# Performance work log

Measured on AMD Instinct MI355X. Metric: run time of the kernel, lower is better.

The kernel has to match this reference:

```python
import jax, jax.numpy as jnp
import numpy as np

N_NODES = 100000
N_EDGES = 3200000
LEAKY_SLOPE = 0.01  # torch F.leaky_relu default


def _conv(x, W, b, src, dst):
    # DGL-style custom GCN conv: sum-aggregate neighbor features, then linear.
    msgs = x[src]                                            # [E, d_in]
    agg = jax.ops.segment_sum(msgs, dst, num_segments=N_NODES)  # [N, d_in]
    return agg @ W + b                                       # [N, d_out]


def setup_inputs() -> dict:
    key = jax.random.key(0)
    ks = jax.random.split(key, 8)
    features = jax.random.normal(ks[0], (N_NODES, 4), dtype=jnp.float32)
    src = jax.random.randint(ks[1], (N_EDGES,), 0, N_NODES, dtype=jnp.int32)
    dst = jax.random.randint(ks[2], (N_EDGES,), 0, N_NODES, dtype=jnp.int32)
    # Kaiming-ish init scale
    W1 = jax.random.normal(ks[3], (4, 64), dtype=jnp.float32) * (1.0 / np.sqrt(4))
    b1 = jnp.zeros((64,), dtype=jnp.float32)
    W2 = jax.random.normal(ks[4], (64, 64), dtype=jnp.float32) * (1.0 / np.sqrt(64))
    b2 = jnp.zeros((64,), dtype=jnp.float32)
    W5 = jax.random.normal(ks[5], (64, 3), dtype=jnp.float32) * (1.0 / np.sqrt(64))
    b5 = jnp.zeros((3,), dtype=jnp.float32)
    return {"features": features, "src": src, "dst": dst,
            "W1": W1, "b1": b1, "W2": W2, "b2": b2, "W5": W5, "b5": b5}


def reference(features, src, dst, W1, b1, W2, b2, W5, b5):
    lrelu = lambda v: jax.nn.leaky_relu(v, negative_slope=LEAKY_SLOPE)
    x = lrelu(_conv(features, W1, b1, src, dst))
    # layer2 weights are shared across 7 applications (as in the torch module)
    for _ in range(7):
        x = lrelu(_conv(x, W2, b2, src, dst))
    x = _conv(x, W5, b5, src, dst)
    return x
```

## Files before the change

### kernel.cpp

```cpp
#include <hip/hip_runtime.h>

#define N_NODES 100000
#define N_EDGES 3200000
#define SLOPE 0.01f

#define NBUCK 391
#define NBLK_B 256
#define EPB (N_EDGES / NBLK_B)
#define NGH (NBUCK * NBLK_B)
#define CAP_C 10240

typedef __attribute__((ext_vector_type(8))) short short8;
typedef __attribute__((ext_vector_type(4))) float f32x4;

static inline size_t align_up(size_t x, size_t a){ return (x + a - 1) / a * a; }

__device__ inline unsigned short f2bf(float f){
  unsigned u = __float_as_uint(f);
  u += 0x7fffu + ((u >> 16) & 1u);
  return (unsigned short)(u >> 16);
}
__device__ inline float bf2f(unsigned short s){
  return __uint_as_float(((unsigned)s) << 16);
}
__device__ inline void add2(float& a0, float& a1, unsigned u){
  a0 += __uint_as_float(u << 16);
  a1 += __uint_as_float(u & 0xffff0000u);
}


__global__ void gbhist_k(const int* __restrict__ dst, int* __restrict__ ghist){
  __shared__ int h[NBUCK];
  int tid = threadIdx.x, blk = blockIdx.x;
  for (int i = tid; i < NBUCK; i += 1024) h[i] = 0;
  __syncthreads();
  int e0 = blk * EPB;
  for (int e = e0 + tid; e < e0 + EPB; e += 1024) atomicAdd(&h[dst[e] >> 8], 1);
  __syncthreads();
  for (int i = tid; i < NBUCK; i += 1024) ghist[i * NBLK_B + blk] = h[i];
}

__global__ void scan1_k(const int* __restrict__ in, int* __restrict__ out,
                        int* __restrict__ bsums, int n){
  __shared__ int lds[256];
  int tid = threadIdx.x;
  int base = blockIdx.x * 1024 + tid * 4;
  int v0 = (base + 0 < n) ? in[base + 0] : 0;
  int v1 = (base + 1 < n) ? in[base + 1] : 0;
  int v2 = (base + 2 < n) ? in[base + 2] : 0;
  int v3 = (base + 3 < n) ? in[base + 3] : 0;
  int tsum = v0 + v1 + v2 + v3;
  lds[tid] = tsum;
  for (int off = 1; off < 256; off <<= 1){
    __syncthreads();
    int x = (tid >= off) ? lds[tid - off] : 0;
    __syncthreads();
    lds[tid] += x;
  }
  __syncthreads();
  int excl = lds[tid] - tsum;
  if (base + 0 < n) out[base + 0] = excl;
  if (base + 1 < n) out[base + 1] = excl + v0;
  if (base + 2 < n) out[base + 2] = excl + v0 + v1;
  if (base + 3 < n) out[base + 3] = excl + v0 + v1 + v2;
  if (tid == 255) bsums[blockIdx.x] = lds[255];
}

__global__ void scan2_k(int* bsums, int nb){
  int lane = threadIdx.x;
  int base = 0;
  for (int off = 0; off < nb; off += 64){
    int idx = off + lane;
    int v = (idx < nb) ? bsums[idx] : 0;
    int sc = v;
    for (int m = 1; m < 64; m <<= 1){
      int t = __shfl_up(sc, m);
      if (lane >= m) sc += t;
    }
    int total = __shfl(sc, 63);
    if (idx < nb) bsums[idx] = sc - v + base;
    base += total;
  }
}

__global__ void scan3_k(int* __restrict__ out, const int* __restrict__ bsums, int n){
  int i = blockIdx.x * 256 + threadIdx.x;
  if (i < n) out[i] += bsums[i >> 10];
}

__global__ void passB_k(const int* __restrict__ src, const int* __restrict__ dst,
                        const int* __restrict__ ghist, const int* __restrict__ goff,
                        int* __restrict__ pk){
  __shared__ int h[NBUCK];
  __shared__ int buf[EPB];
  int tid = threadIdx.x, blk = blockIdx.x;
  for (int i = tid; i < NBUCK; i += 1024) h[i] = ghist[i * NBLK_B + blk];
  __syncthreads();
  if (tid < 64){
    int base = 0;
    for (int off = 0; off < NBUCK; off += 64){
      int idx = off + tid;
      int v = (idx < NBUCK) ? h[idx] : 0;
      int sc = v;
      for (int m = 1; m < 64; m <<= 1){
        int t = __shfl_up(sc, m);
        if (tid >= m) sc += t;
      }
      int total = __shfl(sc, 63);
      if (idx < NBUCK) h[idx] = sc - v + base;
      base += total;
    }
  }
  __syncthreads();
  int e0 = blk * EPB;
  for (int e = e0 + tid; e < e0 + EPB; e += 1024){
    int d = dst[e];
    int p = atomicAdd(&h[d >> 8], 1);
    buf[p] = (src[e] << 8) | (d & 255);
  }
  __syncthreads();
  int wv = tid >> 6, ln = tid & 63;
  for (int b = wv; b < NBUCK; b += 16){
    int s0 = (b == 0) ? 0 : h[b - 1];
    int L  = h[b] - s0;
    int g0 = goff[b * NBLK_B + blk];
    for (int j = ln; j < L; j += 64) pk[g0 + j] = buf[s0 + j];
  }
}

__global__ void passC_k(const int* __restrict__ pk, const int* __restrict__ goff,
                        int* __restrict__ ssrc, int* __restrict__ row_ptr){
  __shared__ int cur[256];
  __shared__ int buf[CAP_C];
  int b = blockIdx.x, tid = threadIdx.x;
  if (tid < 256) cur[tid] = 0;
  __syncthreads();
  int s = goff[b * NBLK_B];
  int e = (b == NBUCK - 1) ? N_EDGES : goff[(b + 1) * NBLK_B];
  int cnt = e - s;
  for (int i = s + tid; i < e; i += 512) atomicAdd(&cur[pk[i] & 255], 1);
  __syncthreads();
  if (tid < 64){
    int base = 0;
    for (int off = 0; off < 256; off += 64){
      int idx = off + tid;
      int v = cur[idx];
      int sc = v;
      for (int m = 1; m < 64; m <<= 1){
        int t = __shfl_up(sc, m);
        if (tid >= m) sc += t;
      }
      int total = __shfl(sc, 63);
      cur[idx] = sc - v + base;
      base += total;
    }
  }
  __syncthreads();
  int node = b * 256 + tid;
  if (tid < 256 && node < N_NODES) row_ptr[node] = s + cur[tid];
  if (b == NBUCK - 1 && tid == 0) row_ptr[N_NODES] = N_EDGES;
  __syncthreads();
  for (int i = s + tid; i < e; i += 512){
    int v = pk[i];
    int p = atomicAdd(&cur[v & 255], 1);
    if (p < CAP_C) buf[p] = v >> 8;
    else ssrc[s + p] = v >> 8;
  }
  __syncthreads();
  int lim = (cnt < CAP_C) ? cnt : CAP_C;
  for (int i = tid; i < lim; i += 512) ssrc[s + i] = buf[i];
}

__global__ void conv1_k(const float* __restrict__ feat, const int* __restrict__ row_ptr,
                        const int* __restrict__ ssrc, const float* __restrict__ W1,
                        const float* __restrict__ b1, unsigned short* __restrict__ out){
  int gt = blockIdx.x * 256 + threadIdx.x;
  int node = gt >> 6;
  int lane = threadIdx.x & 63;
  int s = row_ptr[node], t = row_ptr[node + 1];
  float a0 = 0.f, a1 = 0.f, a2 = 0.f, a3 = 0.f;
  for (int i = s + lane; i < t; i += 64){
    int nb = ssrc[i];
    const float4 v = *(const float4*)(feat + (size_t)nb * 4);
    a0 += v.x; a1 += v.y; a2 += v.z; a3 += v.w;
  }
  for (int m = 1; m < 64; m <<= 1){
    a0 += __shfl_xor(a0, m);
    a1 += __shfl_xor(a1, m);
    a2 += __shfl_xor(a2, m);
    a3 += __shfl_xor(a3, m);
  }
  float o = b1[lane] + a0 * W1[lane] + a1 * W1[64 + lane] + a2 * W1[128 + lane] + a3 * W1[192 + lane];
  o = (o > 0.f) ? o : SLOPE * o;
  out[node * 64 + lane] = f2bf(o);
}

__global__ void mm64_k(const unsigned short* __restrict__ x, const float* __restrict__ W,
                       unsigned short* __restrict__ z){
  int lane = threadIdx.x & 63;
  int wid = (blockIdx.x * blockDim.x + threadIdx.x) >> 6;
  int nwaves = (gridDim.x * blockDim.x) >> 6;
  int r = lane & 15, g = lane >> 4;
  short8 Af[4][2];
  #pragma unroll
  for (int mb = 0; mb < 4; ++mb)
    #pragma unroll
    for (int kt = 0; kt < 2; ++kt){
      short8 f;
      #pragma unroll
      for (int j = 0; j < 8; ++j){
        int k = kt * 32 + g * 8 + j;
        f[j] = (short)f2bf(W[k * 64 + mb * 16 + r]);
      }
      Af[mb][kt] = f;
    }
  const int NT = N_NODES / 16;
  for (int t = wid; t < NT; t += nwaves){
    int base = t * 16;
    const short8 B0 = *(const short8*)(x + (size_t)(base + r) * 64 + g * 8);
    const short8 B1 = *(const short8*)(x + (size_t)(base + r) * 64 + 32 + g * 8);
    #pragma unroll
    for (int mb = 0; mb < 4; ++mb){
      f32x4 c = {0.f, 0.f, 0.f, 0.f};
      c = __builtin_amdgcn_mfma_f32_16x16x32_bf16(Af[mb][0], B0, c, 0, 0, 0);
      c = __builtin_amdgcn_mfma_f32_16x16x32_bf16(Af[mb][1], B1, c, 0, 0, 0);
      ushort4 pk4;
      pk4.x = f2bf(c[0]); pk4.y = f2bf(c[1]); pk4.z = f2bf(c[2]); pk4.w = f2bf(c[3]);
      *(ushort4*)(z + (size_t)(base + r) * 64 + mb * 16 + g * 4) = pk4;
    }
  }
}

__global__ void agg64_k(const unsigned short* __restrict__ z, const int* __restrict__ row_ptr,
                        const int* __restrict__ ssrc, const float* __restrict__ b,
                        unsigned short* __restrict__ out){
  int gt = blockIdx.x * 256 + threadIdx.x;
  int node = gt >> 6;
  int lane = threadIdx.x & 63;
  int s = row_ptr[node], cnt = row_ptr[node + 1] - s;
  int nb_l = ssrc[s + lane];
  int q = lane >> 3, o = lane & 7;
  const size_t oo = (size_t)(o << 3);
  float a0=0.f,a1=0.f,a2=0.f,a3=0.f,a4=0.f,a5=0.f,a6=0.f,a7=0.f;
  int cm1 = (cnt > 0) ? cnt - 1 : 0;
  uint4 v0, v1, v2, v3, v4, v5;
  if (cnt >  0){ int n = __shfl(nb_l, min( 0 + q, cm1)); v0 = *(const uint4*)(z + (size_t)n * 64 + oo); }
  if (cnt >  8){ int n = __shfl(nb_l, min( 8 + q, cm1)); v1 = *(const uint4*)(z + (size_t)n * 64 + oo); }
  if (cnt > 16){ int n = __shfl(nb_l, min(16 + q, cm1)); v2 = *(const uint4*)(z + (size_t)n * 64 + oo); }
  if (cnt > 24){ int n = __shfl(nb_l, min(24 + q, cm1)); v3 = *(const uint4*)(z + (size_t)n * 64 + oo); }
  if (cnt > 32){ int n = __shfl(nb_l, min(32 + q, cm1)); v4 = *(const uint4*)(z + (size_t)n * 64 + oo); }
  if (cnt > 40){ int n = __shfl(nb_l, min(40 + q, cm1)); v5 = *(const uint4*)(z + (size_t)n * 64 + oo); }
  #define ACC(V) { add2(a0,a1,V.x); add2(a2,a3,V.y); add2(a4,a5,V.z); add2(a6,a7,V.w); }
  if (cnt >  0){ if (cnt >=  8) ACC(v0) else { if ( 0 + q < cnt) ACC(v0) } }
  if (cnt >  8){ if (cnt >= 16) ACC(v1) else { if ( 8 + q < cnt) ACC(v1) } }
  if (cnt > 16){ if (cnt >= 24) ACC(v2) else { if (16 + q < cnt) ACC(v2) } }
  if (cnt > 24){ if (cnt >= 32) ACC(v3) else { if (24 + q < cnt) ACC(v3) } }
  if (cnt > 32){ if (cnt >= 40) ACC(v4) else { if (32 + q < cnt) ACC(v4) } }
  if (cnt > 40){ if (cnt >= 48) ACC(v5) else { if (40 + q < cnt) ACC(v5) } }
  #undef ACC
  for (int i = 48 + q; i < cnt; i += 8){
    int nb = ssrc[s + i];
    uint4 vv = *(const uint4*)(z + (size_t)nb * 64 + oo);
    add2(a0,a1,vv.x); add2(a2,a3,vv.y); add2(a4,a5,vv.z); add2(a6,a7,vv.w);
  }
  for (int m = 8; m < 64; m <<= 1){
    a0 += __shfl_xor(a0, m); a1 += __shfl_xor(a1, m);
    a2 += __shfl_xor(a2, m); a3 += __shfl_xor(a3, m);
    a4 += __shfl_xor(a4, m); a5 += __shfl_xor(a5, m);
    a6 += __shfl_xor(a6, m); a7 += __shfl_xor(a7, m);
  }
  if (lane < 8){
    const float4 bA = *(const float4*)(b + lane * 8);
    const float4 bB = *(const float4*)(b + lane * 8 + 4);
    float y0 = a0 + bA.x, y1 = a1 + bA.y, y2 = a2 + bA.z, y3 = a3 + bA.w;
    float y4 = a4 + bB.x, y5 = a5 + bB.y, y6 = a6 + bB.z, y7 = a7 + bB.w;
    y0 = (y0 > 0.f) ? y0 : SLOPE * y0;  y1 = (y1 > 0.f) ? y1 : SLOPE * y1;
    y2 = (y2 > 0.f) ? y2 : SLOPE * y2;  y3 = (y3 > 0.f) ? y3 : SLOPE * y3;
    y4 = (y4 > 0.f) ? y4 : SLOPE * y4;  y5 = (y5 > 0.f) ? y5 : SLOPE * y5;
    y6 = (y6 > 0.f) ? y6 : SLOPE * y6;  y7 = (y7 > 0.f) ? y7 : SLOPE * y7;
    uint4 pkd;
    pkd.x = (unsigned)f2bf(y0) | ((unsigned)f2bf(y1) << 16);
    pkd.y = (unsigned)f2bf(y2) | ((unsigned)f2bf(y3) << 16);
    pkd.z = (unsigned)f2bf(y4) | ((unsigned)f2bf(y5) << 16);
    pkd.w = (unsigned)f2bf(y6) | ((unsigned)f2bf(y7) << 16);
    *(uint4*)(out + (size_t)node * 64 + lane * 8) = pkd;
  }
}

__global__ void premult_k(const unsigned short* __restrict__ x, const float* __restrict__ W5,
                          float* __restrict__ y4){
  int gt = blockIdx.x * 256 + threadIdx.x;
  int node = gt >> 6;
  int lane = threadIdx.x & 63;
  float xv = bf2f(x[node * 64 + lane]);
  float p0 = xv * W5[lane * 3 + 0];
  float p1 = xv * W5[lane * 3 + 1];
  float p2 = xv * W5[lane * 3 + 2];
  for (int m = 1; m < 64; m <<= 1){
    p0 += __shfl_xor(p0, m);
    p1 += __shfl_xor(p1, m);
    p2 += __shfl_xor(p2, m);
  }
  if (lane == 0){
    float4 v; v.x = p0; v.y = p1; v.z = p2; v.w = 0.f;
    *(float4*)(y4 + (size_t)node * 4) = v;
  }
}

__global__ void agg3_k(const float* __restrict__ y4, const int* __restrict__ row_ptr,
                       const int* __restrict__ ssrc, const float* __restrict__ b5,
                       float* __restrict__ out){
  int gt = blockIdx.x * 256 + threadIdx.x;
  int node = gt >> 6;
  int lane = threadIdx.x & 63;
  int s = row_ptr[node], t = row_ptr[node + 1];
  int c = lane & 3;
  float acc = 0.f;
  for (int i = s + (lane >> 2); i < t; i += 16) acc += y4[(size_t)ssrc[i] * 4 + c];
  for (int m = 4; m < 64; m <<= 1) acc += __shfl_xor(acc, m);
  if (lane < 3) out[node * 3 + lane] = acc + b5[lane];
}


extern "C" void kernel_launch(void* const* d_in, const int* in_sizes, int n_in,
                              void* d_out, int out_size, void* d_ws, size_t ws_size,
                              hipStream_t stream){
  const float* feat = (const float*)d_in[0];
  const int*   src  = (const int*)d_in[1];
  const int*   dst  = (const int*)d_in[2];
  const float* W1   = (const float*)d_in[3];
  const float* b1   = (const float*)d_in[4];
  const float* W2   = (const float*)d_in[5];
  const float* b2   = (const float*)d_in[6];
  const float* W5   = (const float*)d_in[7];
  const float* b5   = (const float*)d_in[8];
  float* out = (float*)d_out;

  char* p = (char*)d_ws;
  auto carve = [&](size_t bytes) -> char* {
    char* r = p; p += align_up(bytes, 512); return r;
  };
  int*   row_ptr = (int*)carve((size_t)(N_NODES + 1) * 4);
  int*   bsums   = (int*)carve(512 * 4);
  int*   ghist   = (int*)carve((size_t)NGH * 4);
  int*   goff    = (int*)carve((size_t)NGH * 4);
  int*   ssrc    = (int*)carve(((size_t)N_EDGES + 64) * 4);
  unsigned short* bufA = (unsigned short*)carve((size_t)N_NODES * 64 * 2);
  unsigned short* bufB = (unsigned short*)carve((size_t)N_NODES * 64 * 2);
  float* y4      = (float*)carve((size_t)N_NODES * 4 * 4);
  int*   pk      = (int*)carve((size_t)N_EDGES * 4);
  unsigned short* zbuf = (unsigned short*)pk;

  gbhist_k<<<NBLK_B, 1024, 0, stream>>>(dst, ghist);
  {
    int nb = (NGH + 1023) / 1024;
    scan1_k<<<nb, 256, 0, stream>>>(ghist, goff, bsums, NGH);
    scan2_k<<<1, 64, 0, stream>>>(bsums, nb);
    scan3_k<<<(NGH + 255) / 256, 256, 0, stream>>>(goff, bsums, NGH);
  }
  passB_k<<<NBLK_B, 1024, 0, stream>>>(src, dst, ghist, goff, pk);
  passC_k<<<NBUCK, 512, 0, stream>>>(pk, goff, ssrc, row_ptr);
  hipMemsetAsync(ssrc + N_EDGES, 0, 64 * 4, stream);

  conv1_k<<<(N_NODES * 64) / 256, 256, 0, stream>>>(feat, row_ptr, ssrc, W1, b1, bufA);

  unsigned short* xin = bufA;
  unsigned short* xout = bufB;
  for (int l = 0; l < 7; ++l){
    mm64_k<<<512, 256, 0, stream>>>(xin, W2, zbuf);
    agg64_k<<<(N_NODES * 64) / 256, 256, 0, stream>>>(zbuf, row_ptr, ssrc, b2, xout);
    unsigned short* tmp = xin; xin = xout; xout = tmp;
  }

  premult_k<<<(N_NODES * 64) / 256, 256, 0, stream>>>(xin, W5, y4);
  agg3_k<<<(N_NODES * 64) / 256, 256, 0, stream>>>(y4, row_ptr, ssrc, b5, out);
}
```

Baseline: 606.5 us.

## Fuse aggregation and 64x64 MFMA matmul into one kernel per layer

Replaces the per-layer matmul-then-aggregate kernel pair with a single kernel that first gathers and sums neighbour rows, then multiplies the 16-node tile by W2 with MFMA from shared memory and applies bias plus leaky ReLU. The intermediate z buffer and one launch per layer go away. W2 is converted once into a bf16 fragment layout by a small precompute kernel. The neighbour loads are also made unconditional and clamped so they can all issue together. The cost is that only one wave of each 1024-thread block runs the MFMA after a barrier, and rounding the aggregate to bf16 before the matmul changes numerics slightly.

```diff
diff --git a/kernel.cpp b/kernel.cpp
--- a/kernel.cpp
+++ b/kernel.cpp
@@ -171,6 +171,17 @@
   for (int i = tid; i < lim; i += 512) ssrc[s + i] = buf[i];
 }
 
+__global__ void wfrag_k(const float* __restrict__ W, unsigned short* __restrict__ Wfrag){
+  int l = threadIdx.x;
+  int r = l & 15, g = l >> 4;
+  for (int mb = 0; mb < 4; ++mb)
+    for (int kt = 0; kt < 2; ++kt)
+      for (int j = 0; j < 8; ++j){
+        int k = kt * 32 + g * 8 + j;
+        Wfrag[((mb * 2 + kt) * 64 + l) * 8 + j] = f2bf(W[k * 64 + mb * 16 + r]);
+      }
+}
+
 __global__ void conv1_k(const float* __restrict__ feat, const int* __restrict__ row_ptr,
                         const int* __restrict__ ssrc, const float* __restrict__ W1,
                         const float* __restrict__ b1, unsigned short* __restrict__ out){
@@ -195,72 +206,42 @@
   out[node * 64 + lane] = f2bf(o);
 }
 
-__global__ void mm64_k(const unsigned short* __restrict__ x, const float* __restrict__ W,
-                       unsigned short* __restrict__ z){
-  int lane = threadIdx.x & 63;
-  int wid = (blockIdx.x * blockDim.x + threadIdx.x) >> 6;
-  int nwaves = (gridDim.x * blockDim.x) >> 6;
-  int r = lane & 15, g = lane >> 4;
-  short8 Af[4][2];
-  #pragma unroll
-  for (int mb = 0; mb < 4; ++mb)
-    #pragma unroll
-    for (int kt = 0; kt < 2; ++kt){
-      short8 f;
-      #pragma unroll
-      for (int j = 0; j < 8; ++j){
-        int k = kt * 32 + g * 8 + j;
-        f[j] = (short)f2bf(W[k * 64 + mb * 16 + r]);
-      }
-      Af[mb][kt] = f;
-    }
-  const int NT = N_NODES / 16;
-  for (int t = wid; t < NT; t += nwaves){
-    int base = t * 16;
-    const short8 B0 = *(const short8*)(x + (size_t)(base + r) * 64 + g * 8);
-    const short8 B1 = *(const short8*)(x + (size_t)(base + r) * 64 + 32 + g * 8);
-    #pragma unroll
-    for (int mb = 0; mb < 4; ++mb){
-      f32x4 c = {0.f, 0.f, 0.f, 0.f};
-      c = __builtin_amdgcn_mfma_f32_16x16x32_bf16(Af[mb][0], B0, c, 0, 0, 0);
-      c = __builtin_amdgcn_mfma_f32_16x16x32_bf16(Af[mb][1], B1, c, 0, 0, 0);
-      ushort4 pk4;
-      pk4.x = f2bf(c[0]); pk4.y = f2bf(c[1]); pk4.z = f2bf(c[2]); pk4.w = f2bf(c[3]);
-      *(ushort4*)(z + (size_t)(base + r) * 64 + mb * 16 + g * 4) = pk4;
-    }
-  }
-}
-
-__global__ void agg64_k(const unsigned short* __restrict__ z, const int* __restrict__ row_ptr,
-                        const int* __restrict__ ssrc, const float* __restrict__ b,
-                        unsigned short* __restrict__ out){
-  int gt = blockIdx.x * 256 + threadIdx.x;
-  int node = gt >> 6;
-  int lane = threadIdx.x & 63;
+__global__ __launch_bounds__(1024) void aggmm_k(
+    const unsigned short* __restrict__ x, const int* __restrict__ row_ptr,
+    const int* __restrict__ ssrc, const unsigned short* __restrict__ Wfrag,
+    const float* __restrict__ b, unsigned short* __restrict__ out){
+  __shared__ unsigned short aggL[16][72];
+  int tid = threadIdx.x;
+  int w = tid >> 6, lane = tid & 63;
+  int node = blockIdx.x * 16 + w;
   int s = row_ptr[node], cnt = row_ptr[node + 1] - s;
   int nb_l = ssrc[s + lane];
   int q = lane >> 3, o = lane & 7;
   const size_t oo = (size_t)(o << 3);
   float a0=0.f,a1=0.f,a2=0.f,a3=0.f,a4=0.f,a5=0.f,a6=0.f,a7=0.f;
+  uint4 v0, v1, v2, v3, v4, v5;
   int cm1 = (cnt > 0) ? cnt - 1 : 0;
-  uint4 v0, v1, v2, v3, v4, v5;
-  if (cnt >  0){ int n = __shfl(nb_l, min( 0 + q, cm1)); v0 = *(const uint4*)(z + (size_t)n * 64 + oo); }
-  if (cnt >  8){ int n = __shfl(nb_l, min( 8 + q, cm1)); v1 = *(const uint4*)(z + (size_t)n * 64 + oo); }
-  if (cnt > 16){ int n = __shfl(nb_l, min(16 + q, cm1)); v2 = *(const uint4*)(z + (size_t)n * 64 + oo); }
-  if (cnt > 24){ int n = __shfl(nb_l, min(24 + q, cm1)); v3 = *(const uint4*)(z + (size_t)n * 64 + oo); }
-  if (cnt > 32){ int n = __shfl(nb_l, min(32 + q, cm1)); v4 = *(const uint4*)(z + (size_t)n * 64 + oo); }
-  if (cnt > 40){ int n = __shfl(nb_l, min(40 + q, cm1)); v5 = *(const uint4*)(z + (size_t)n * 64 + oo); }
-  #define ACC(V) { add2(a0,a1,V.x); add2(a2,a3,V.y); add2(a4,a5,V.z); add2(a6,a7,V.w); }
-  if (cnt >  0){ if (cnt >=  8) ACC(v0) else { if ( 0 + q < cnt) ACC(v0) } }
-  if (cnt >  8){ if (cnt >= 16) ACC(v1) else { if ( 8 + q < cnt) ACC(v1) } }
-  if (cnt > 16){ if (cnt >= 24) ACC(v2) else { if (16 + q < cnt) ACC(v2) } }
-  if (cnt > 24){ if (cnt >= 32) ACC(v3) else { if (24 + q < cnt) ACC(v3) } }
-  if (cnt > 32){ if (cnt >= 40) ACC(v4) else { if (32 + q < cnt) ACC(v4) } }
-  if (cnt > 40){ if (cnt >= 48) ACC(v5) else { if (40 + q < cnt) ACC(v5) } }
-  #undef ACC
+  {
+    int j0 = min( 0 + q, cm1), j1 = min( 8 + q, cm1), j2 = min(16 + q, cm1);
+    int j3 = min(24 + q, cm1), j4 = min(32 + q, cm1), j5 = min(40 + q, cm1);
+    int n0 = __shfl(nb_l, j0), n1 = __shfl(nb_l, j1), n2 = __shfl(nb_l, j2);
+    int n3 = __shfl(nb_l, j3), n4 = __shfl(nb_l, j4), n5 = __shfl(nb_l, j5);
+    v0 = *(const uint4*)(x + (size_t)n0 * 64 + oo);
+    v1 = *(const uint4*)(x + (size_t)n1 * 64 + oo);
+    v2 = *(const uint4*)(x + (size_t)n2 * 64 + oo);
+    v3 = *(const uint4*)(x + (size_t)n3 * 64 + oo);
+    v4 = *(const uint4*)(x + (size_t)n4 * 64 + oo);
+    v5 = *(const uint4*)(x + (size_t)n5 * 64 + oo);
+  }
+  if ( 0 + q < cnt){ add2(a0,a1,v0.x); add2(a2,a3,v0.y); add2(a4,a5,v0.z); add2(a6,a7,v0.w); }
+  if ( 8 + q < cnt){ add2(a0,a1,v1.x); add2(a2,a3,v1.y); add2(a4,a5,v1.z); add2(a6,a7,v1.w); }
+  if (16 + q < cnt){ add2(a0,a1,v2.x); add2(a2,a3,v2.y); add2(a4,a5,v2.z); add2(a6,a7,v2.w); }
+  if (24 + q < cnt){ add2(a0,a1,v3.x); add2(a2,a3,v3.y); add2(a4,a5,v3.z); add2(a6,a7,v3.w); }
+  if (32 + q < cnt){ add2(a0,a1,v4.x); add2(a2,a3,v4.y); add2(a4,a5,v4.z); add2(a6,a7,v4.w); }
+  if (40 + q < cnt){ add2(a0,a1,v5.x); add2(a2,a3,v5.y); add2(a4,a5,v5.z); add2(a6,a7,v5.w); }
   for (int i = 48 + q; i < cnt; i += 8){
     int nb = ssrc[s + i];
-    uint4 vv = *(const uint4*)(z + (size_t)nb * 64 + oo);
+    uint4 vv = *(const uint4*)(x + (size_t)nb * 64 + oo);
     add2(a0,a1,vv.x); add2(a2,a3,vv.y); add2(a4,a5,vv.z); add2(a6,a7,vv.w);
   }
   for (int m = 8; m < 64; m <<= 1){
@@ -270,20 +251,34 @@
     a6 += __shfl_xor(a6, m); a7 += __shfl_xor(a7, m);
   }
   if (lane < 8){
-    const float4 bA = *(const float4*)(b + lane * 8);
-    const float4 bB = *(const float4*)(b + lane * 8 + 4);
-    float y0 = a0 + bA.x, y1 = a1 + bA.y, y2 = a2 + bA.z, y3 = a3 + bA.w;
-    float y4 = a4 + bB.x, y5 = a5 + bB.y, y6 = a6 + bB.z, y7 = a7 + bB.w;
-    y0 = (y0 > 0.f) ? y0 : SLOPE * y0;  y1 = (y1 > 0.f) ? y1 : SLOPE * y1;
-    y2 = (y2 > 0.f) ? y2 : SLOPE * y2;  y3 = (y3 > 0.f) ? y3 : SLOPE * y3;
-    y4 = (y4 > 0.f) ? y4 : SLOPE * y4;  y5 = (y5 > 0.f) ? y5 : SLOPE * y5;
-    y6 = (y6 > 0.f) ? y6 : SLOPE * y6;  y7 = (y7 > 0.f) ? y7 : SLOPE * y7;
     uint4 pkd;
-    pkd.x = (unsigned)f2bf(y0) | ((unsigned)f2bf(y1) << 16);
-    pkd.y = (unsigned)f2bf(y2) | ((unsigned)f2bf(y3) << 16);
-    pkd.z = (unsigned)f2bf(y4) | ((unsigned)f2bf(y5) << 16);
-    pkd.w = (unsigned)f2bf(y6) | ((unsigned)f2bf(y7) << 16);
-    *(uint4*)(out + (size_t)node * 64 + lane * 8) = pkd;
+    pkd.x = (unsigned)f2bf(a0) | ((unsigned)f2bf(a1) << 16);
+    pkd.y = (unsigned)f2bf(a2) | ((unsigned)f2bf(a3) << 16);
+    pkd.z = (unsigned)f2bf(a4) | ((unsigned)f2bf(a5) << 16);
+    pkd.w = (unsigned)f2bf(a6) | ((unsigned)f2bf(a7) << 16);
+    *(uint4*)&aggL[w][lane * 8] = pkd;
+  }
+  __syncthreads();
+  if (w == 0){
+    int r = lane & 15, g = lane >> 4;
+    const short8* Wf = (const short8*)Wfrag;
+    const short8 B0 = *(const short8*)&aggL[r][g * 8];
+    const short8 B1 = *(const short8*)&aggL[r][32 + g * 8];
+    #pragma unroll
+    for (int mb = 0; mb < 4; ++mb){
+      f32x4 c = {0.f, 0.f, 0.f, 0.f};
+      c = __builtin_amdgcn_mfma_f32_16x16x32_bf16(Wf[(mb * 2 + 0) * 64 + lane], B0, c, 0, 0, 0);
+      c = __builtin_amdgcn_mfma_f32_16x16x32_bf16(Wf[(mb * 2 + 1) * 64 + lane], B1, c, 0, 0, 0);
+      const float4 bb = *(const float4*)(b + mb * 16 + g * 4);
+      float y0 = c[0] + bb.x, y1 = c[1] + bb.y, y2 = c[2] + bb.z, y3 = c[3] + bb.w;
+      y0 = (y0 > 0.f) ? y0 : SLOPE * y0;
+      y1 = (y1 > 0.f) ? y1 : SLOPE * y1;
+      y2 = (y2 > 0.f) ? y2 : SLOPE * y2;
+      y3 = (y3 > 0.f) ? y3 : SLOPE * y3;
+      ushort4 pk4;
+      pk4.x = f2bf(y0); pk4.y = f2bf(y1); pk4.z = f2bf(y2); pk4.w = f2bf(y3);
+      *(ushort4*)(out + (size_t)(blockIdx.x * 16 + r) * 64 + mb * 16 + g * 4) = pk4;
+    }
   }
 }
 
@@ -342,6 +337,7 @@
   };
   int*   row_ptr = (int*)carve((size_t)(N_NODES + 1) * 4);
   int*   bsums   = (int*)carve(512 * 4);
+  unsigned short* Wfrag = (unsigned short*)carve(4096 * 2);
   int*   ghist   = (int*)carve((size_t)NGH * 4);
   int*   goff    = (int*)carve((size_t)NGH * 4);
   int*   ssrc    = (int*)carve(((size_t)N_EDGES + 64) * 4);
@@ -349,7 +345,6 @@
   unsigned short* bufB = (unsigned short*)carve((size_t)N_NODES * 64 * 2);
   float* y4      = (float*)carve((size_t)N_NODES * 4 * 4);
   int*   pk      = (int*)carve((size_t)N_EDGES * 4);
-  unsigned short* zbuf = (unsigned short*)pk;
 
   gbhist_k<<<NBLK_B, 1024, 0, stream>>>(dst, ghist);
   {
@@ -361,14 +356,14 @@
   passB_k<<<NBLK_B, 1024, 0, stream>>>(src, dst, ghist, goff, pk);
   passC_k<<<NBUCK, 512, 0, stream>>>(pk, goff, ssrc, row_ptr);
   hipMemsetAsync(ssrc + N_EDGES, 0, 64 * 4, stream);
+  wfrag_k<<<1, 64, 0, stream>>>(W2, Wfrag);
 
   conv1_k<<<(N_NODES * 64) / 256, 256, 0, stream>>>(feat, row_ptr, ssrc, W1, b1, bufA);
 
   unsigned short* xin = bufA;
   unsigned short* xout = bufB;
   for (int l = 0; l < 7; ++l){
-    mm64_k<<<512, 256, 0, stream>>>(xin, W2, zbuf);
-    agg64_k<<<(N_NODES * 64) / 256, 256, 0, stream>>>(zbuf, row_ptr, ssrc, b2, xout);
+    aggmm_k<<<N_NODES / 16, 1024, 0, stream>>>(xin, row_ptr, ssrc, Wfrag, b2, xout);
     unsigned short* tmp = xin; xin = xout; xout = tmp;
   }
 
```

Measured after the change: 555.0 us. 8.5% less time.

## Split node features into two 32-wide halves and aggregate each half separately

Applied to the files above, without the earlier changes.

Stores the 64-feature bf16 node arrays as two 32-column planes, with the matmul writing both halves and two aggregation launches per layer each gathering one half. The aim is to shrink the random-gather working set per pass so it fits better in cache. It also precomputes the bf16 MFMA fragments of W2 once in a small kernel instead of converting in every wave. The cost is reading the edge index list twice per layer, extra launches, and narrower per-lane gathers.

```diff
diff --git a/kernel.cpp b/kernel.cpp
--- a/kernel.cpp
+++ b/kernel.cpp
@@ -171,9 +171,21 @@
   for (int i = tid; i < lim; i += 512) ssrc[s + i] = buf[i];
 }
 
+__global__ void wfrag_k(const float* __restrict__ W, unsigned short* __restrict__ Wfrag){
+  int l = threadIdx.x;
+  int r = l & 15, g = l >> 4;
+  for (int mb = 0; mb < 4; ++mb)
+    for (int kt = 0; kt < 2; ++kt)
+      for (int j = 0; j < 8; ++j){
+        int k = kt * 32 + g * 8 + j;
+        Wfrag[((mb * 2 + kt) * 64 + l) * 8 + j] = f2bf(W[k * 64 + mb * 16 + r]);
+      }
+}
+
 __global__ void conv1_k(const float* __restrict__ feat, const int* __restrict__ row_ptr,
                         const int* __restrict__ ssrc, const float* __restrict__ W1,
-                        const float* __restrict__ b1, unsigned short* __restrict__ out){
+                        const float* __restrict__ b1,
+                        unsigned short* __restrict__ outA, unsigned short* __restrict__ outB){
   int gt = blockIdx.x * 256 + threadIdx.x;
   int node = gt >> 6;
   int lane = threadIdx.x & 63;
@@ -192,33 +204,29 @@
   }
   float o = b1[lane] + a0 * W1[lane] + a1 * W1[64 + lane] + a2 * W1[128 + lane] + a3 * W1[192 + lane];
   o = (o > 0.f) ? o : SLOPE * o;
-  out[node * 64 + lane] = f2bf(o);
-}
-
-__global__ void mm64_k(const unsigned short* __restrict__ x, const float* __restrict__ W,
-                       unsigned short* __restrict__ z){
+  if (lane < 32) outA[node * 32 + lane] = f2bf(o);
+  else           outB[node * 32 + lane - 32] = f2bf(o);
+}
+
+__global__ void mm64_k(const unsigned short* __restrict__ xA, const unsigned short* __restrict__ xB,
+                       const unsigned short* __restrict__ Wfrag,
+                       unsigned short* __restrict__ zA, unsigned short* __restrict__ zB){
   int lane = threadIdx.x & 63;
   int wid = (blockIdx.x * blockDim.x + threadIdx.x) >> 6;
   int nwaves = (gridDim.x * blockDim.x) >> 6;
   int r = lane & 15, g = lane >> 4;
+  const short8* Wf = (const short8*)Wfrag;
   short8 Af[4][2];
   #pragma unroll
-  for (int mb = 0; mb < 4; ++mb)
-    #pragma unroll
-    for (int kt = 0; kt < 2; ++kt){
-      short8 f;
-      #pragma unroll
-      for (int j = 0; j < 8; ++j){
-        int k = kt * 32 + g * 8 + j;
-        f[j] = (short)f2bf(W[k * 64 + mb * 16 + r]);
-      }
-      Af[mb][kt] = f;
-    }
+  for (int mb = 0; mb < 4; ++mb){
+    Af[mb][0] = Wf[(mb * 2 + 0) * 64 + lane];
+    Af[mb][1] = Wf[(mb * 2 + 1) * 64 + lane];
+  }
   const int NT = N_NODES / 16;
   for (int t = wid; t < NT; t += nwaves){
     int base = t * 16;
-    const short8 B0 = *(const short8*)(x + (size_t)(base + r) * 64 + g * 8);
-    const short8 B1 = *(const short8*)(x + (size_t)(base + r) * 64 + 32 + g * 8);
+    const short8 B0 = *(const short8*)(xA + (size_t)(base + r) * 32 + g * 8);
+    const short8 B1 = *(const short8*)(xB + (size_t)(base + r) * 32 + g * 8);
     #pragma unroll
     for (int mb = 0; mb < 4; ++mb){
       f32x4 c = {0.f, 0.f, 0.f, 0.f};
@@ -226,73 +234,72 @@
       c = __builtin_amdgcn_mfma_f32_16x16x32_bf16(Af[mb][1], B1, c, 0, 0, 0);
       ushort4 pk4;
       pk4.x = f2bf(c[0]); pk4.y = f2bf(c[1]); pk4.z = f2bf(c[2]); pk4.w = f2bf(c[3]);
-      *(ushort4*)(z + (size_t)(base + r) * 64 + mb * 16 + g * 4) = pk4;
+      unsigned short* dst = (mb < 2)
+        ? (zA + (size_t)(base + r) * 32 + mb * 16 + g * 4)
+        : (zB + (size_t)(base + r) * 32 + (mb - 2) * 16 + g * 4);
+      *(ushort4*)dst = pk4;
     }
   }
 }
 
-__global__ void agg64_k(const unsigned short* __restrict__ z, const int* __restrict__ row_ptr,
-                        const int* __restrict__ ssrc, const float* __restrict__ b,
-                        unsigned short* __restrict__ out){
+__global__ void aggH_k(const unsigned short* __restrict__ z, const int* __restrict__ row_ptr,
+                       const int* __restrict__ ssrc, const float* __restrict__ b32,
+                       unsigned short* __restrict__ outp){
   int gt = blockIdx.x * 256 + threadIdx.x;
   int node = gt >> 6;
   int lane = threadIdx.x & 63;
   int s = row_ptr[node], cnt = row_ptr[node + 1] - s;
   int nb_l = ssrc[s + lane];
   int q = lane >> 3, o = lane & 7;
-  const size_t oo = (size_t)(o << 3);
-  float a0=0.f,a1=0.f,a2=0.f,a3=0.f,a4=0.f,a5=0.f,a6=0.f,a7=0.f;
+  const size_t oo = (size_t)(o << 2);
+  float a0=0.f,a1=0.f,a2=0.f,a3=0.f;
+  uint2 v0, v1, v2, v3, v4, v5;
   int cm1 = (cnt > 0) ? cnt - 1 : 0;
-  uint4 v0, v1, v2, v3, v4, v5;
-  if (cnt >  0){ int n = __shfl(nb_l, min( 0 + q, cm1)); v0 = *(const uint4*)(z + (size_t)n * 64 + oo); }
-  if (cnt >  8){ int n = __shfl(nb_l, min( 8 + q, cm1)); v1 = *(const uint4*)(z + (size_t)n * 64 + oo); }
-  if (cnt > 16){ int n = __shfl(nb_l, min(16 + q, cm1)); v2 = *(const uint4*)(z + (size_t)n * 64 + oo); }
-  if (cnt > 24){ int n = __shfl(nb_l, min(24 + q, cm1)); v3 = *(const uint4*)(z + (size_t)n * 64 + oo); }
-  if (cnt > 32){ int n = __shfl(nb_l, min(32 + q, cm1)); v4 = *(const uint4*)(z + (size_t)n * 64 + oo); }
-  if (cnt > 40){ int n = __shfl(nb_l, min(40 + q, cm1)); v5 = *(const uint4*)(z + (size_t)n * 64 + oo); }
-  #define ACC(V) { add2(a0,a1,V.x); add2(a2,a3,V.y); add2(a4,a5,V.z); add2(a6,a7,V.w); }
-  if (cnt >  0){ if (cnt >=  8) ACC(v0) else { if ( 0 + q < cnt) ACC(v0) } }
-  if (cnt >  8){ if (cnt >= 16) ACC(v1) else { if ( 8 + q < cnt) ACC(v1) } }
-  if (cnt > 16){ if (cnt >= 24) ACC(v2) else { if (16 + q < cnt) ACC(v2) } }
-  if (cnt > 24){ if (cnt >= 32) ACC(v3) else { if (24 + q < cnt) ACC(v3) } }
-  if (cnt > 32){ if (cnt >= 40) ACC(v4) else { if (32 + q < cnt) ACC(v4) } }
-  if (cnt > 40){ if (cnt >= 48) ACC(v5) else { if (40 + q < cnt) ACC(v5) } }
-  #undef ACC
+  {
+    int j0 = min( 0 + q, cm1), j1 = min( 8 + q, cm1), j2 = min(16 + q, cm1);
+    int j3 = min(24 + q, cm1), j4 = min(32 + q, cm1), j5 = min(40 + q, cm1);
+    int n0 = __shfl(nb_l, j0), n1 = __shfl(nb_l, j1), n2 = __shfl(nb_l, j2);
+    int n3 = __shfl(nb_l, j3), n4 = __shfl(nb_l, j4), n5 = __shfl(nb_l, j5);
+    v0 = *(const uint2*)(z + (size_t)n0 * 32 + oo);
+    v1 = *(const uint2*)(z + (size_t)n1 * 32 + oo);
+    v2 = *(const uint2*)(z + (size_t)n2 * 32 + oo);
+    v3 = *(const uint2*)(z + (size_t)n3 * 32 + oo);
+    v4 = *(const uint2*)(z + (size_t)n4 * 32 + oo);
+    v5 = *(const uint2*)(z + (size_t)n5 * 32 + oo);
+  }
+  if ( 0 + q < cnt){ add2(a0,a1,v0.x); add2(a2,a3,v0.y); }
+  if ( 8 + q < cnt){ add2(a0,a1,v1.x); add2(a2,a3,v1.y); }
+  if (16 + q < cnt){ add2(a0,a1,v2.x); add2(a2,a3,v2.y); }
+  if (24 + q < cnt){ add2(a0,a1,v3.x); add2(a2,a3,v3.y); }
+  if (32 + q < cnt){ add2(a0,a1,v4.x); add2(a2,a3,v4.y); }
+  if (40 + q < cnt){ add2(a0,a1,v5.x); add2(a2,a3,v5.y); }
   for (int i = 48 + q; i < cnt; i += 8){
     int nb = ssrc[s + i];
-    uint4 vv = *(const uint4*)(z + (size_t)nb * 64 + oo);
-    add2(a0,a1,vv.x); add2(a2,a3,vv.y); add2(a4,a5,vv.z); add2(a6,a7,vv.w);
+    uint2 vv = *(const uint2*)(z + (size_t)nb * 32 + oo);
+    add2(a0,a1,vv.x); add2(a2,a3,vv.y);
   }
   for (int m = 8; m < 64; m <<= 1){
     a0 += __shfl_xor(a0, m); a1 += __shfl_xor(a1, m);
     a2 += __shfl_xor(a2, m); a3 += __shfl_xor(a3, m);
-    a4 += __shfl_xor(a4, m); a5 += __shfl_xor(a5, m);
-    a6 += __shfl_xor(a6, m); a7 += __shfl_xor(a7, m);
   }
   if (lane < 8){
-    const float4 bA = *(const float4*)(b + lane * 8);
-    const float4 bB = *(const float4*)(b + lane * 8 + 4);
-    float y0 = a0 + bA.x, y1 = a1 + bA.y, y2 = a2 + bA.z, y3 = a3 + bA.w;
-    float y4 = a4 + bB.x, y5 = a5 + bB.y, y6 = a6 + bB.z, y7 = a7 + bB.w;
+    const float4 bb = *(const float4*)(b32 + lane * 4);
+    float y0 = a0 + bb.x, y1 = a1 + bb.y, y2 = a2 + bb.z, y3 = a3 + bb.w;
     y0 = (y0 > 0.f) ? y0 : SLOPE * y0;  y1 = (y1 > 0.f) ? y1 : SLOPE * y1;
     y2 = (y2 > 0.f) ? y2 : SLOPE * y2;  y3 = (y3 > 0.f) ? y3 : SLOPE * y3;
-    y4 = (y4 > 0.f) ? y4 : SLOPE * y4;  y5 = (y5 > 0.f) ? y5 : SLOPE * y5;
-    y6 = (y6 > 0.f) ? y6 : SLOPE * y6;  y7 = (y7 > 0.f) ? y7 : SLOPE * y7;
-    uint4 pkd;
+    uint2 pkd;
     pkd.x = (unsigned)f2bf(y0) | ((unsigned)f2bf(y1) << 16);
     pkd.y = (unsigned)f2bf(y2) | ((unsigned)f2bf(y3) << 16);
-    pkd.z = (unsigned)f2bf(y4) | ((unsigned)f2bf(y5) << 16);
-    pkd.w = (unsigned)f2bf(y6) | ((unsigned)f2bf(y7) << 16);
-    *(uint4*)(out + (size_t)node * 64 + lane * 8) = pkd;
-  }
-}
-
-__global__ void premult_k(const unsigned short* __restrict__ x, const float* __restrict__ W5,
-                          float* __restrict__ y4){
+    *(uint2*)(outp + (size_t)node * 32 + lane * 4) = pkd;
+  }
+}
+
+__global__ void premult_k(const unsigned short* __restrict__ xA, const unsigned short* __restrict__ xB,
+                          const float* __restrict__ W5, float* __restrict__ y4){
   int gt = blockIdx.x * 256 + threadIdx.x;
   int node = gt >> 6;
   int lane = threadIdx.x & 63;
-  float xv = bf2f(x[node * 64 + lane]);
+  float xv = (lane < 32) ? bf2f(xA[node * 32 + lane]) : bf2f(xB[node * 32 + lane - 32]);
   float p0 = xv * W5[lane * 3 + 0];
   float p1 = xv * W5[lane * 3 + 1];
   float p2 = xv * W5[lane * 3 + 2];
@@ -342,14 +349,18 @@
   };
   int*   row_ptr = (int*)carve((size_t)(N_NODES + 1) * 4);
   int*   bsums   = (int*)carve(512 * 4);
+  unsigned short* Wfrag = (unsigned short*)carve(4096 * 2);
   int*   ghist   = (int*)carve((size_t)NGH * 4);
   int*   goff    = (int*)carve((size_t)NGH * 4);
   int*   ssrc    = (int*)carve(((size_t)N_EDGES + 64) * 4);
-  unsigned short* bufA = (unsigned short*)carve((size_t)N_NODES * 64 * 2);
-  unsigned short* bufB = (unsigned short*)carve((size_t)N_NODES * 64 * 2);
+  unsigned short* fA0 = (unsigned short*)carve((size_t)N_NODES * 32 * 2);
+  unsigned short* fB0 = (unsigned short*)carve((size_t)N_NODES * 32 * 2);
+  unsigned short* fA1 = (unsigned short*)carve((size_t)N_NODES * 32 * 2);
+  unsigned short* fB1 = (unsigned short*)carve((size_t)N_NODES * 32 * 2);
   float* y4      = (float*)carve((size_t)N_NODES * 4 * 4);
   int*   pk      = (int*)carve((size_t)N_EDGES * 4);
-  unsigned short* zbuf = (unsigned short*)pk;
+  unsigned short* zA = (unsigned short*)pk;
+  unsigned short* zB = zA + (size_t)N_NODES * 32;
 
   gbhist_k<<<NBLK_B, 1024, 0, stream>>>(dst, ghist);
   {
@@ -361,17 +372,20 @@
   passB_k<<<NBLK_B, 1024, 0, stream>>>(src, dst, ghist, goff, pk);
   passC_k<<<NBUCK, 512, 0, stream>>>(pk, goff, ssrc, row_ptr);
   hipMemsetAsync(ssrc + N_EDGES, 0, 64 * 4, stream);
-
-  conv1_k<<<(N_NODES * 64) / 256, 256, 0, stream>>>(feat, row_ptr, ssrc, W1, b1, bufA);
-
-  unsigned short* xin = bufA;
-  unsigned short* xout = bufB;
+  wfrag_k<<<1, 64, 0, stream>>>(W2, Wfrag);
+
+  conv1_k<<<(N_NODES * 64) / 256, 256, 0, stream>>>(feat, row_ptr, ssrc, W1, b1, fA0, fB0);
+
+  unsigned short *xinA = fA0, *xinB = fB0, *xoutA = fA1, *xoutB = fB1;
   for (int l = 0; l < 7; ++l){
-    mm64_k<<<512, 256, 0, stream>>>(xin, W2, zbuf);
-    agg64_k<<<(N_NODES * 64) / 256, 256, 0, stream>>>(zbuf, row_ptr, ssrc, b2, xout);
-    unsigned short* tmp = xin; xin = xout; xout = tmp;
-  }
-
-  premult_k<<<(N_NODES * 64) / 256, 256, 0, stream>>>(xin, W5, y4);
+    mm64_k<<<512, 256, 0, stream>>>(xinA, xinB, Wfrag, zA, zB);
+    aggH_k<<<(N_NODES * 64) / 256, 256, 0, stream>>>(zA, row_ptr, ssrc, b2, xoutA);
+    aggH_k<<<(N_NODES * 64) / 256, 256, 0, stream>>>(zB, row_ptr, ssrc, b2 + 32, xoutB);
+    unsigned short* t;
+    t = xinA; xinA = xoutA; xoutA = t;
+    t = xinB; xinB = xoutB; xoutB = t;
+  }
+
+  premult_k<<<(N_NODES * 64) / 256, 256, 0, stream>>>(xinA, xinB, W5, y4);
   agg3_k<<<(N_NODES * 64) / 256, 256, 0, stream>>>(y4, row_ptr, ssrc, b5, out);
 }
```

New measurement: 736.9 us. 21.5% more time.
